# Kernel optimization log

Measured on AMD Instinct MI355X. Metric: run time of the kernel, lower is better.

Reference implementation:

```python
import jax, jax.numpy as jnp
import numpy as np

ETA = 0.5  # from init_kwargs; eta >= 0 branch
N = 16777216

def setup_inputs() -> dict:
    key = jax.random.key(0)
    k1, k2 = jax.random.split(key)
    outputs = jax.random.normal(k1, (N,), dtype=jnp.float32)
    # PNU targets in {-1, 0, 1}
    targets = jax.random.randint(k2, (N,), 0, 3, dtype=jnp.int32) - 1
    p_ratio = jnp.array([0.4, 0.6], dtype=jnp.float32)
    return {"outputs": outputs, "targets": targets, "p_ratio": p_ratio}

def reference(outputs, targets, p_ratio):
    y = outputs.reshape(-1)
    t = targets.reshape(-1).astype(y.dtype)

    # masks (computed once, fused)
    idx_p = jnp.maximum(t, 0.0)          # positive examples
    idx_n = jnp.maximum(-t, 0.0)         # negative examples
    idx_u = 1.0 - jnp.abs(t)             # unlabeled examples

    sig_neg = jax.nn.sigmoid(-y)         # loss_func(-y)
    sig_pos = jax.nn.sigmoid(y)          # loss_func(-(-y))

    n_p = jnp.maximum(1.0, jnp.sum(idx_p))
    n_n = jnp.maximum(1.0, jnp.sum(idx_n))
    n_u = jnp.maximum(1.0, jnp.sum(idx_u))

    R_P_plus  = jnp.sum(idx_p * sig_neg) / n_p
    R_P_minus = jnp.sum(idx_p * sig_pos) / n_p
    R_N_minus = jnp.sum(idx_n * sig_pos) / n_n
    R_U_minus = jnp.sum(idx_u * sig_pos) / n_u

    R_PN = p_ratio[0] * R_P_plus + p_ratio[1] * R_N_minus
    R_PU = p_ratio[0] * (R_P_plus - R_P_minus) + R_U_minus

    # eta >= 0 branch
    return (1.0 - ETA) * R_PN + ETA * R_PU
```

## Files before the change

kernel.cpp:

```cpp
#include <hip/hip_runtime.h>

#define ETA 0.5f
#define NTHREADS 256
#define UNROLL 4
#define CHUNK (NTHREADS * UNROLL)
#define NACC 5

__device__ __forceinline__ float wave_reduce_sum(float v) {
#pragma unroll
    for (int off = 32; off > 0; off >>= 1)
        v += __shfl_down(v, off, 64);
    return v;
}

__device__ __forceinline__ void pnu_accum(float yy, int tt,
                                          float& sAll, float& sT, float& sA,
                                          float& cT, float& cA) {
    float s = __builtin_amdgcn_rcpf(1.0f + __expf(-yy));
    float tf = (float)tt;
    float ta = fabsf(tf);
    sAll += s;
    sT = fmaf(tf, s, sT);
    sA = fmaf(ta, s, sA);
    cT += tf;
    cA += ta;
}

__global__ __launch_bounds__(NTHREADS) void pnu_partial_kernel(
    const float* __restrict__ y, const int* __restrict__ t,
    float* __restrict__ partials, int n, int nblocks, int nfull) {
    const int nvec = n >> 2;
    const float4* __restrict__ y4 = reinterpret_cast<const float4*>(y);
    const int4* __restrict__ t4 = reinterpret_cast<const int4*>(t);

    float sAll = 0.f, sT = 0.f, sA = 0.f, cT = 0.f, cA = 0.f;

    for (int c = blockIdx.x; c < nfull; c += gridDim.x) {
        const int base = c * CHUNK + threadIdx.x;
        float4 yv[UNROLL];
        int4 tv[UNROLL];
#pragma unroll
        for (int u = 0; u < UNROLL; ++u) yv[u] = y4[base + u * NTHREADS];
#pragma unroll
        for (int u = 0; u < UNROLL; ++u) tv[u] = t4[base + u * NTHREADS];
#pragma unroll
        for (int u = 0; u < UNROLL; ++u) {
            pnu_accum(yv[u].x, tv[u].x, sAll, sT, sA, cT, cA);
            pnu_accum(yv[u].y, tv[u].y, sAll, sT, sA, cT, cA);
            pnu_accum(yv[u].z, tv[u].z, sAll, sT, sA, cT, cA);
            pnu_accum(yv[u].w, tv[u].w, sAll, sT, sA, cT, cA);
        }
    }

    if (blockIdx.x == gridDim.x - 1) {
        for (int i = nfull * CHUNK + threadIdx.x; i < nvec; i += NTHREADS) {
            float4 yv = y4[i];
            int4 tv = t4[i];
            pnu_accum(yv.x, tv.x, sAll, sT, sA, cT, cA);
            pnu_accum(yv.y, tv.y, sAll, sT, sA, cT, cA);
            pnu_accum(yv.z, tv.z, sAll, sT, sA, cT, cA);
            pnu_accum(yv.w, tv.w, sAll, sT, sA, cT, cA);
        }
        for (int i = (nvec << 2) + threadIdx.x; i < n; i += NTHREADS)
            pnu_accum(y[i], t[i], sAll, sT, sA, cT, cA);
    }

    float vals[NACC] = {sAll, sT, sA, cT, cA};
    __shared__ float red[NTHREADS / 64][NACC];
    const int lane = threadIdx.x & 63;
    const int wave = threadIdx.x >> 6;
#pragma unroll
    for (int k = 0; k < NACC; ++k) {
        float r = wave_reduce_sum(vals[k]);
        if (lane == 0) red[wave][k] = r;
    }
    __syncthreads();
    if (threadIdx.x < NACC) {
        float r = 0.f;
#pragma unroll
        for (int w = 0; w < NTHREADS / 64; ++w) r += red[w][threadIdx.x];
        partials[threadIdx.x * nblocks + blockIdx.x] = r;
    }
}

#define FTHREADS 1024

__global__ __launch_bounds__(FTHREADS) void pnu_final_kernel(
    const float* __restrict__ partials, const float* __restrict__ p_ratio,
    float* __restrict__ out, int nblocks, int n) {
    float acc[NACC] = {0.f, 0.f, 0.f, 0.f, 0.f};
    for (int i = threadIdx.x; i < nblocks; i += FTHREADS) {
#pragma unroll
        for (int k = 0; k < NACC; ++k) acc[k] += partials[k * nblocks + i];
    }
    __shared__ float red[FTHREADS / 64][NACC];
    const int lane = threadIdx.x & 63;
    const int wave = threadIdx.x >> 6;
#pragma unroll
    for (int k = 0; k < NACC; ++k) {
        float r = wave_reduce_sum(acc[k]);
        if (lane == 0) red[wave][k] = r;
    }
    __syncthreads();
    if (threadIdx.x == 0) {
        float tot[NACC];
#pragma unroll
        for (int k = 0; k < NACC; ++k) {
            float r = 0.f;
#pragma unroll
            for (int w = 0; w < FTHREADS / 64; ++w) r += red[w][k];
            tot[k] = r;
        }
        const float sAll = tot[0], sT = tot[1], sA = tot[2];
        const float cT = tot[3], cA = tot[4];

        const float cP = 0.5f * (cA + cT);
        const float cN = 0.5f * (cA - cT);
        const float cU = (float)n - cA;
        const float sPm = 0.5f * (sA + sT);
        const float sNm = 0.5f * (sA - sT);
        const float sUm = sAll - sA;
        const float sPp = cP - sPm;

        const float nP = fmaxf(1.0f, cP);
        const float nN = fmaxf(1.0f, cN);
        const float nU = fmaxf(1.0f, cU);

        const float R_P_plus  = sPp / nP;
        const float R_P_minus = sPm / nP;
        const float R_N_minus = sNm / nN;
        const float R_U_minus = sUm / nU;

        const float pi0 = p_ratio[0], pi1 = p_ratio[1];
        const float R_PN = pi0 * R_P_plus + pi1 * R_N_minus;
        const float R_PU = pi0 * (R_P_plus - R_P_minus) + R_U_minus;

        out[0] = (1.0f - ETA) * R_PN + ETA * R_PU;
    }
}

extern "C" void kernel_launch(void* const* d_in, const int* in_sizes, int n_in,
                              void* d_out, int out_size, void* d_ws, size_t ws_size,
                              hipStream_t stream) {
    const float* y = (const float*)d_in[0];
    const int* t = (const int*)d_in[1];
    const float* p_ratio = (const float*)d_in[2];
    float* out = (float*)d_out;
    float* partials = (float*)d_ws;

    const int n = in_sizes[0];
    const int nvec = n >> 2;
    const int nfull = nvec / CHUNK;
    const bool tail = (nfull * CHUNK * 4) < n;
    int nblocks = nfull + (tail ? 1 : 0);
    if (nblocks < 1) nblocks = 1;

    int maxblocks = (int)(ws_size / (NACC * sizeof(float)));
    if (maxblocks < 1) maxblocks = 1;
    if (nblocks > maxblocks) nblocks = maxblocks;

    pnu_partial_kernel<<<nblocks, NTHREADS, 0, stream>>>(y, t, partials, n, nblocks, nfull);
    pnu_final_kernel<<<1, FTHREADS, 0, stream>>>(partials, p_ratio, out, nblocks, n);
}
```

Measured before the change: 30.43 us.

## Give each block contiguous chunks with double-buffered register prefetch

Each block now handles several contiguous chunks (four by default) instead of one, so the grid and the partials array shrink by about four times. Inside a block, the loads for the next chunk are issued into a second register buffer before the current chunk is computed, which overlaps memory latency with the sigmoid math. The cost is higher register pressure from the two buffers (launch bounds now ask for 4 blocks per SM) and fewer blocks overall, which may leave less parallelism to hide latency.

Result: no change. 29.89 us, median of 2 (-1.8%).

```diff
diff --git a/kernel.cpp b/kernel.cpp
--- a/kernel.cpp
+++ b/kernel.cpp
@@ -4,6 +4,7 @@
 #define NTHREADS 256
 #define UNROLL 4
 #define CHUNK (NTHREADS * UNROLL)
+#define NCHUNKS 4
 #define NACC 5
 
 __device__ __forceinline__ float wave_reduce_sum(float v) {
@@ -26,29 +27,51 @@
     cA += ta;
 }
 
-__global__ __launch_bounds__(NTHREADS) void pnu_partial_kernel(
+#define LOAD_CHUNK(YB, TB, c)                                                \
+    do {                                                                     \
+        const int base_ = (c) * CHUNK + threadIdx.x;                         \
+        _Pragma("unroll")                                                    \
+        for (int u = 0; u < UNROLL; ++u) YB[u] = y4[base_ + u * NTHREADS];   \
+        _Pragma("unroll")                                                    \
+        for (int u = 0; u < UNROLL; ++u) TB[u] = t4[base_ + u * NTHREADS];   \
+    } while (0)
+
+#define COMPUTE_CHUNK(YB, TB)                                                \
+    do {                                                                     \
+        _Pragma("unroll")                                                    \
+        for (int u = 0; u < UNROLL; ++u) {                                   \
+            pnu_accum(YB[u].x, TB[u].x, sAll, sT, sA, cT, cA);               \
+            pnu_accum(YB[u].y, TB[u].y, sAll, sT, sA, cT, cA);               \
+            pnu_accum(YB[u].z, TB[u].z, sAll, sT, sA, cT, cA);               \
+            pnu_accum(YB[u].w, TB[u].w, sAll, sT, sA, cT, cA);               \
+        }                                                                    \
+    } while (0)
+
+__global__ __launch_bounds__(NTHREADS, 4) void pnu_partial_kernel(
     const float* __restrict__ y, const int* __restrict__ t,
-    float* __restrict__ partials, int n, int nblocks, int nfull) {
+    float* __restrict__ partials, int n, int nblocks, int nfull, int cpb) {
     const int nvec = n >> 2;
     const float4* __restrict__ y4 = reinterpret_cast<const float4*>(y);
     const int4* __restrict__ t4 = reinterpret_cast<const int4*>(t);
 
     float sAll = 0.f, sT = 0.f, sA = 0.f, cT = 0.f, cA = 0.f;
 
-    for (int c = blockIdx.x; c < nfull; c += gridDim.x) {
-        const int base = c * CHUNK + threadIdx.x;
-        float4 yv[UNROLL];
-        int4 tv[UNROLL];
-#pragma unroll
-        for (int u = 0; u < UNROLL; ++u) yv[u] = y4[base + u * NTHREADS];
-#pragma unroll
-        for (int u = 0; u < UNROLL; ++u) tv[u] = t4[base + u * NTHREADS];
-#pragma unroll
-        for (int u = 0; u < UNROLL; ++u) {
-            pnu_accum(yv[u].x, tv[u].x, sAll, sT, sA, cT, cA);
-            pnu_accum(yv[u].y, tv[u].y, sAll, sT, sA, cT, cA);
-            pnu_accum(yv[u].z, tv[u].z, sAll, sT, sA, cT, cA);
-            pnu_accum(yv[u].w, tv[u].w, sAll, sT, sA, cT, cA);
+    {
+        int c = blockIdx.x * cpb;
+        int end = c + cpb;
+        if (end > nfull) end = nfull;
+        if (c < end) {
+            float4 yvA[UNROLL], yvB[UNROLL];
+            int4 tvA[UNROLL], tvB[UNROLL];
+            LOAD_CHUNK(yvA, tvA, c);
+            while (c + 2 <= end) {
+                LOAD_CHUNK(yvB, tvB, c + 1);
+                COMPUTE_CHUNK(yvA, tvA);
+                if (c + 2 < end) LOAD_CHUNK(yvA, tvA, c + 2);
+                COMPUTE_CHUNK(yvB, tvB);
+                c += 2;
+            }
+            if (c < end) COMPUTE_CHUNK(yvA, tvA);
         }
     }
 
@@ -152,13 +175,18 @@
     const int nvec = n >> 2;
     const int nfull = nvec / CHUNK;
     const bool tail = (nfull * CHUNK * 4) < n;
-    int nblocks = nfull + (tail ? 1 : 0);
+
+    int nblocks = (nfull + NCHUNKS - 1) / NCHUNKS;
+    if (tail && nblocks < 1) nblocks = 1;
     if (nblocks < 1) nblocks = 1;
 
     int maxblocks = (int)(ws_size / (NACC * sizeof(float)));
     if (maxblocks < 1) maxblocks = 1;
     if (nblocks > maxblocks) nblocks = maxblocks;
 
-    pnu_partial_kernel<<<nblocks, NTHREADS, 0, stream>>>(y, t, partials, n, nblocks, nfull);
+    const int cpb = (nfull + nblocks - 1) / nblocks;
+
+    pnu_partial_kernel<<<nblocks, NTHREADS, 0, stream>>>(y, t, partials, n,
+                                                         nblocks, nfull, cpb);
     pnu_final_kernel<<<1, FTHREADS, 0, stream>>>(partials, p_ratio, out, nblocks, n);
 }
```
